# Performance work log

Measured on AMD Instinct MI355X. Metric: run time of the kernel, lower is better.

The kernel has to match this reference:

```python
import jax, jax.numpy as jnp
import numpy as np

D_STATE = 16
D_CONV = 4
DT_RANK = 16  # ceil(d_model/16) = ceil(256/16)
N_LAYERS = 2
EPS = 1e-5


def _layernorm(x, g, b):
    m = jnp.mean(x, -1, keepdims=True)
    v = jnp.var(x, -1, keepdims=True)
    return (x - m) * jax.lax.rsqrt(v + EPS) * g + b


def _causal_conv(x, w, b):
    # x [B,L,D], depthwise causal conv, w [D,K], b [D]
    K = w.shape[1]
    L = x.shape[1]
    xp = jnp.pad(x, ((0, 0), (K - 1, 0), (0, 0)))
    y = sum(xp[:, k:k + L, :] * w[:, k] for k in range(K))
    return y + b


def _selective_scan(u, dt, A, Bm, Cm, D_skip):
    # u, dt [B,L,d]; A [d,n]; Bm, Cm [B,L,n]; D_skip [d]
    def step(h, inp):
        dt_t, B_t, C_t, u_t = inp  # [B,d],[B,n],[B,n],[B,d]
        dA = jnp.exp(dt_t[:, :, None] * A)                      # [B,d,n]
        h = dA * h + dt_t[:, :, None] * B_t[:, None, :] * u_t[:, :, None]
        y = jnp.einsum('bdn,bn->bd', h, C_t)
        return h, y

    Bsz, L, d = u.shape
    h0 = jnp.zeros((Bsz, d, A.shape[1]), u.dtype)
    xs = (dt.transpose(1, 0, 2), Bm.transpose(1, 0, 2),
          Cm.transpose(1, 0, 2), u.transpose(1, 0, 2))
    _, ys = jax.lax.scan(step, h0, xs)                          # [L,B,d]
    return ys.transpose(1, 0, 2) + u * D_skip


def _mamba_block(x, Wip, cw, cb, Wxp, Wdt, bdt, Alog, Dp, Wout):
    xz = x @ Wip                                                # [B,L,2*d_inner]
    d_inner = Wip.shape[1] // 2
    xc, z = xz[..., :d_inner], xz[..., d_inner:]
    xc = jax.nn.silu(_causal_conv(xc, cw, cb))
    xdbl = xc @ Wxp                                             # [B,L,dt_rank+2n]
    dt = jax.nn.softplus(xdbl[..., :DT_RANK] @ Wdt + bdt)
    Bm = xdbl[..., DT_RANK:DT_RANK + D_STATE]
    Cm = xdbl[..., DT_RANK + D_STATE:]
    A = -jnp.exp(Alog)
    y = _selective_scan(xc, dt, A, Bm, Cm, Dp)
    y = y * jax.nn.silu(z)
    return y @ Wout


def reference(z_t, W_in, b_in, ln_g, ln_b, W_inproj, conv_w, conv_b, W_xproj,
              W_dt, b_dt, A_log, D_skip, W_out, W_outp, b_outp, lno_g, lno_b):
    x = z_t @ W_in + b_in                                       # [B,L,d_model]
    for i in range(N_LAYERS):
        res = x
        xn = _layernorm(x, ln_g[i], ln_b[i])
        x = res + _mamba_block(xn, W_inproj[i], conv_w[i], conv_b[i],
                               W_xproj[i], W_dt[i], b_dt[i], A_log[i],
                               D_skip[i], W_out[i])  # dropout is identity in eval
    u = x @ W_outp + b_outp
    return _layernorm(u, lno_g, lno_b)


def setup_inputs() -> dict:
    key = jax.random.key(0)
    B, L = 16, 2048
    d_input, d_model, d_output, d_inner = 1088, 256, 64, 512
    n = N_LAYERS
    ks = jax.random.split(key, 10)

    def rn(k, shape, fan):
        return jax.random.normal(k, shape, jnp.float32) / np.float32(np.sqrt(fan))

    A_init = jnp.log(jnp.arange(1, D_STATE + 1, dtype=jnp.float32))
    return {
        'z_t': jax.random.normal(ks[0], (B, L, d_input), jnp.float32),
        'W_in': rn(ks[1], (d_input, d_model), d_input),
        'b_in': jnp.zeros((d_model,), jnp.float32),
        'ln_g': jnp.ones((n, d_model), jnp.float32),
        'ln_b': jnp.zeros((n, d_model), jnp.float32),
        'W_inproj': rn(ks[2], (n, d_model, 2 * d_inner), d_model),
        'conv_w': rn(ks[3], (n, d_inner, D_CONV), D_CONV),
        'conv_b': jnp.zeros((n, d_inner), jnp.float32),
        'W_xproj': rn(ks[4], (n, d_inner, DT_RANK + 2 * D_STATE), d_inner),
        'W_dt': rn(ks[5], (n, DT_RANK, d_inner), DT_RANK),
        'b_dt': jnp.full((n, d_inner), -4.6, jnp.float32),  # softplus ~ 0.01
        'A_log': jnp.broadcast_to(A_init, (n, d_inner, D_STATE)) + 0.0,
        'D_skip': jnp.ones((n, d_inner), jnp.float32),
        'W_out': rn(ks[6], (n, d_inner, d_model), d_inner),
        'W_outp': rn(ks[7], (d_model, d_output), d_model),
        'b_outp': jnp.zeros((d_output,), jnp.float32),
        'lno_g': jnp.ones((d_output,), jnp.float32),
        'lno_b': jnp.zeros((d_output,), jnp.float32),
    }
```

## Files before the change

kernel.cpp:

```cpp
#include <hip/hip_runtime.h>
#include <hip/hip_bf16.h>
#include <math.h>
#include <stdint.h>

#define L_SEQ 2048
#define BATCH 16
#define NROWS (BATCH * L_SEQ)
#define DMODEL 256
#define DINNER 512
#define C_CH 32
#define T_CH 64
#define LOG2E 1.4426950408889634f

typedef __attribute__((ext_vector_type(8))) __bf16 bf16x8;
typedef __attribute__((ext_vector_type(4))) float f32x4;
typedef __attribute__((ext_vector_type(8))) unsigned short u16x8;
typedef __attribute__((address_space(1))) const uint32_t gu32;
typedef __attribute__((address_space(3))) uint32_t lu32;

#if __has_builtin(__builtin_amdgcn_exp2f)
#define EXP2F __builtin_amdgcn_exp2f
#else
#define EXP2F exp2f
#endif

__device__ __forceinline__ float sigmoidf_(float x) { return 1.f / (1.f + __expf(-x)); }

__device__ __forceinline__ unsigned short f2bf(float f) {
    union { float f; uint32_t u; } v; v.f = f;
    uint32_t r = v.u + 0x7FFF + ((v.u >> 16) & 1);
    return (unsigned short)(r >> 16);
}
__device__ __forceinline__ float bf2f(unsigned short h) {
    union { uint32_t u; float f; } v; v.u = ((uint32_t)h) << 16;
    return v.f;
}

__device__ __forceinline__ void gld16(const void* g, void* l) {
    __builtin_amdgcn_global_load_lds((gu32*)g, (lu32*)l, 16, 0, 0);
}

__global__ __launch_bounds__(256) void wtrans(const float* __restrict__ W,
                                              unsigned short* __restrict__ Wt, int K, int N) {
    int idx = blockIdx.x * 256 + threadIdx.x;
    if (idx < K * N) {
        int n = idx / K, k = idx % K;
        Wt[idx] = f2bf(W[(size_t)k * N + n]);
    }
}
__global__ __launch_bounds__(256) void wtrans_pad(const float* __restrict__ W,
                                                  unsigned short* __restrict__ Wt,
                                                  int K, int Nreal, int Npad) {
    int idx = blockIdx.x * 256 + threadIdx.x;
    if (idx < Npad * K) {
        int n = idx / K, k = idx % K;
        Wt[idx] = (n < Nreal) ? f2bf(W[(size_t)k * Nreal + n]) : (unsigned short)0;
    }
}

template <int TM, bool A_F32, bool HAS_BIAS, bool HAS_RES, bool OUT_BF16>
__global__ __launch_bounds__(256) void gemm_bf16(
    const void* __restrict__ Aptr, const unsigned short* __restrict__ Bt,
    const float* __restrict__ bias, const float* __restrict__ res,
    void* __restrict__ Cout, int M, int N, int K, int Nout)
{
    constexpr int MR = TM / 32;
    __shared__ unsigned short Alds[2][TM * 32];
    __shared__ unsigned short Blds[2][4096];
    const int tid = threadIdx.x;
    const int w = tid >> 6, lane = tid & 63;

    const int nwg = gridDim.x;
    const int q = nwg >> 3;
    const int wg = (blockIdx.x & 7) * q + (blockIdx.x >> 3);
    const int nx = N >> 7;
    const int bm = (wg / nx) * TM, bn = (wg % nx) * 128;

    const int wr = (w >> 1) * (TM / 2), wc = (w & 1) * 64;
    const int fr = lane & 15, fq = lane >> 4;
    const size_t Kb = (size_t)K * 2;

    const int o0 = tid * 16, o1 = (256 + tid) * 16;
    const int ar0 = o0 >> 6, ac0 = o0 & 63;
    const int ar1 = o1 >> 6, ac1 = o1 & 63;
    const char* Ab = (const char*)Aptr;
    const float* Af = (const float*)Aptr;
    const char* Bb = (const char*)Bt;
    const int lds0 = w * 1024, lds1 = 4096 + w * 1024;

    f32x4 acc[MR][4];
#pragma unroll
    for (int m = 0; m < MR; m++)
#pragma unroll
        for (int n = 0; n < 4; n++) acc[m][n] = (f32x4){0.f, 0.f, 0.f, 0.f};

    auto stageB = [&](int buf, int k0) {
        char* lB = (char*)Blds[buf];
        gld16(Bb + (size_t)(bn + ar0) * Kb + (k0 << 1) + ac0, lB + lds0);
        gld16(Bb + (size_t)(bn + ar1) * Kb + (k0 << 1) + ac1, lB + lds1);
    };
    auto stageA16 = [&](int buf, int k0) {
        char* lA = (char*)Alds[buf];
        gld16(Ab + (size_t)(bm + ar0) * Kb + (k0 << 1) + ac0, lA + lds0);
        if constexpr (TM == 128)
            gld16(Ab + (size_t)(bm + ar1) * Kb + (k0 << 1) + ac1, lA + lds1);
    };
    float4 r00, r01, r10, r11;
    auto loadA32 = [&](int k0) {
        const float* s0 = Af + (size_t)(bm + ar0) * K + k0 + (ac0 >> 1);
        r00 = *(const float4*)s0; r01 = *(const float4*)(s0 + 4);
        if constexpr (TM == 128) {
            const float* s1 = Af + (size_t)(bm + ar1) * K + k0 + (ac1 >> 1);
            r10 = *(const float4*)s1; r11 = *(const float4*)(s1 + 4);
        }
    };
    auto writeA32 = [&](int buf) {
        bf16x8 v0;
        v0[0]=(__bf16)r00.x; v0[1]=(__bf16)r00.y; v0[2]=(__bf16)r00.z; v0[3]=(__bf16)r00.w;
        v0[4]=(__bf16)r01.x; v0[5]=(__bf16)r01.y; v0[6]=(__bf16)r01.z; v0[7]=(__bf16)r01.w;
        *(bf16x8*)((char*)Alds[buf] + ar0 * 64 + ac0) = v0;
        if constexpr (TM == 128) {
            bf16x8 v1;
            v1[0]=(__bf16)r10.x; v1[1]=(__bf16)r10.y; v1[2]=(__bf16)r10.z; v1[3]=(__bf16)r10.w;
            v1[4]=(__bf16)r11.x; v1[5]=(__bf16)r11.y; v1[6]=(__bf16)r11.z; v1[7]=(__bf16)r11.w;
            *(bf16x8*)((char*)Alds[buf] + ar1 * 64 + ac1) = v1;
        }
    };
    auto compute = [&](int buf) {
        bf16x8 af[MR], bg[4];
#pragma unroll
        for (int m = 0; m < MR; m++)
            af[m] = *(const bf16x8*)&Alds[buf][(wr + m * 16 + fr) * 32 + fq * 8];
#pragma unroll
        for (int n = 0; n < 4; n++)
            bg[n] = *(const bf16x8*)&Blds[buf][(wc + n * 16 + fr) * 32 + fq * 8];
#pragma unroll
        for (int m = 0; m < MR; m++)
#pragma unroll
            for (int n = 0; n < 4; n++)
                acc[m][n] = __builtin_amdgcn_mfma_f32_16x16x32_bf16(af[m], bg[n], acc[m][n], 0, 0, 0);
    };

    if constexpr (A_F32) { loadA32(0); stageB(0, 0); writeA32(0); }
    else                 { stageA16(0, 0); stageB(0, 0); }
    asm volatile("s_waitcnt vmcnt(0) lgkmcnt(0)" ::: "memory");
    __builtin_amdgcn_s_barrier();
    __builtin_amdgcn_sched_barrier(0);

    const int NT = K >> 5;
    for (int kt = 0; kt < NT; ++kt) {
        const int cur = kt & 1;
        const bool has_next = (kt + 1 < NT);
        if (has_next) {
            const int k0 = (kt + 1) << 5;
            if constexpr (A_F32) { loadA32(k0); stageB(cur ^ 1, k0); }
            else                 { stageA16(cur ^ 1, k0); stageB(cur ^ 1, k0); }
        }
        if (has_next) {
            if constexpr (A_F32 && TM == 128)      asm volatile("s_waitcnt vmcnt(6)" ::: "memory");
            else if constexpr (A_F32)              asm volatile("s_waitcnt vmcnt(4)" ::: "memory");
            else if constexpr (TM == 128)          asm volatile("s_waitcnt vmcnt(4)" ::: "memory");
            else                                   asm volatile("s_waitcnt vmcnt(3)" ::: "memory");
        } else {
            asm volatile("s_waitcnt vmcnt(0)" ::: "memory");
        }
        __builtin_amdgcn_s_barrier();
        __builtin_amdgcn_sched_barrier(0);

        compute(cur);
        if constexpr (A_F32) { if (has_next) writeA32(cur ^ 1); }

        asm volatile("s_waitcnt lgkmcnt(0)" ::: "memory");
        __builtin_amdgcn_s_barrier();
        __builtin_amdgcn_sched_barrier(0);
    }

#pragma unroll
    for (int m = 0; m < MR; m++) {
#pragma unroll
        for (int n = 0; n < 4; n++) {
            int col = bn + wc + n * 16 + fr;
            if (col < Nout) {
#pragma unroll
                for (int r = 0; r < 4; r++) {
                    int row = bm + wr + m * 16 + fq * 4 + r;
                    float v = acc[m][n][r];
                    if (HAS_BIAS) v += bias[col];
                    if (HAS_RES)  v += res[(size_t)row * Nout + col];
                    if (OUT_BF16) ((unsigned short*)Cout)[(size_t)row * Nout + col] = f2bf(v);
                    else          ((float*)Cout)[(size_t)row * Nout + col] = v;
                }
            }
        }
    }
}

__global__ __launch_bounds__(256) void ln256(
    const float* __restrict__ x, const float* __restrict__ g,
    const float* __restrict__ b, unsigned short* __restrict__ out)
{
    int lane = threadIdx.x & 63, wid = threadIdx.x >> 6;
    size_t r = (size_t)blockIdx.x * 4 + wid;
    const float4 v = *(const float4*)&x[r * 256 + lane * 4];
    float s = v.x + v.y + v.z + v.w;
    float sq = v.x * v.x + v.y * v.y + v.z * v.z + v.w * v.w;
#pragma unroll
    for (int off = 32; off; off >>= 1) { s += __shfl_xor(s, off); sq += __shfl_xor(sq, off); }
    float mean = s * (1.f / 256.f);
    float var = sq * (1.f / 256.f) - mean * mean;
    float rs = rsqrtf(var + 1e-5f);
    float4 gv = *(const float4*)&g[lane * 4];
    float4 bv = *(const float4*)&b[lane * 4];
    ushort4 o;
    o.x = f2bf((v.x - mean) * rs * gv.x + bv.x);
    o.y = f2bf((v.y - mean) * rs * gv.y + bv.y);
    o.z = f2bf((v.z - mean) * rs * gv.z + bv.z);
    o.w = f2bf((v.w - mean) * rs * gv.w + bv.w);
    *(ushort4*)&out[r * 256 + lane * 4] = o;
}

__global__ __launch_bounds__(256) void ln64(
    const float* __restrict__ t, const float* __restrict__ g,
    const float* __restrict__ b, float* __restrict__ out)
{
    int lane = threadIdx.x & 63, wid = threadIdx.x >> 6;
    size_t r = (size_t)blockIdx.x * 4 + wid;
    float v = t[r * 64 + lane];
    float s = v, sq = v * v;
#pragma unroll
    for (int off = 32; off; off >>= 1) { s += __shfl_xor(s, off); sq += __shfl_xor(sq, off); }
    float mean = s * (1.f / 64.f);
    float var = sq * (1.f / 64.f) - mean * mean;
    out[r * 64 + lane] = (v - mean) * rsqrtf(var + 1e-5f) * g[lane] + b[lane];
}

__global__ __launch_bounds__(256) void conv_silu8(
    const unsigned short* __restrict__ xz, const float* __restrict__ w,
    const float* __restrict__ cb, unsigned short* __restrict__ xc)
{
    int idx = blockIdx.x * 256 + threadIdx.x;
    int d8 = (idx & 63) << 3;
    int l  = (idx >> 6) & 2047;
    int b  = idx >> 17;
    const unsigned short* base = xz + ((size_t)b * L_SEQ + l) * 1024 + d8;
    u16x8 t0 = {0,0,0,0,0,0,0,0}, t1 = t0, t2 = t0;
    u16x8 t3 = *(const u16x8*)base;
    if (l >= 1) t2 = *(const u16x8*)(base - 1024);
    if (l >= 2) t1 = *(const u16x8*)(base - 2048);
    if (l >= 3) t0 = *(const u16x8*)(base - 3072);
    u16x8 o;
#pragma unroll
    for (int j = 0; j < 8; j++) {
        float4 wv = *(const float4*)&w[(d8 + j) * 4];
        float acc = cb[d8 + j];
        acc = fmaf(bf2f(t0[j]), wv.x, acc);
        acc = fmaf(bf2f(t1[j]), wv.y, acc);
        acc = fmaf(bf2f(t2[j]), wv.z, acc);
        acc = fmaf(bf2f(t3[j]), wv.w, acc);
        o[j] = f2bf(acc * sigmoidf_(acc));
    }
    *(u16x8*)&xc[((size_t)b * L_SEQ + l) * 512 + d8] = o;
}

__global__ __launch_bounds__(256) void dt_kernel(
    const float* __restrict__ xdbl, const float* __restrict__ Wdt,
    const float* __restrict__ bdt, unsigned short* __restrict__ dtb)
{
    int idx = blockIdx.x * 256 + threadIdx.x;
    int d = idx & 511;
    int rblk = idx >> 9;
    float wdt[16];
#pragma unroll
    for (int j = 0; j < 16; j++) wdt[j] = Wdt[j * 512 + d];
    const float bd = bdt[d];
#pragma unroll
    for (int i = 0; i < 8; i++) {
        size_t r = (size_t)rblk * 8 + i;
        const float* xr = xdbl + r * 48;
        float p0 = 0.f, p1 = 0.f, p2 = 0.f, p3 = 0.f;
#pragma unroll
        for (int j = 0; j < 4; j++) {
            p0 = fmaf(xr[j],      wdt[j],      p0);
            p1 = fmaf(xr[4 + j],  wdt[4 + j],  p1);
            p2 = fmaf(xr[8 + j],  wdt[8 + j],  p2);
            p3 = fmaf(xr[12 + j], wdt[12 + j], p3);
        }
        float dtr = bd + ((p0 + p1) + (p2 + p3));
        float dtv = (dtr > 20.f) ? dtr : __logf(1.f + __expf(dtr));
        dtb[r * 512 + d] = f2bf(dtv);
    }
}

__global__ __launch_bounds__(256) void scan_pass1(
    const unsigned short* __restrict__ xc, const unsigned short* __restrict__ dtb,
    const float* __restrict__ xdbl, const float* __restrict__ Alog,
    float* __restrict__ Pbuf, float* __restrict__ Sbuf)
{
    __shared__ float xsB[T_CH][16];
    int idx = blockIdx.x * 256 + threadIdx.x;
    int d = idx & 511;
    int c = (idx >> 9) & (C_CH - 1);
    int b = idx >> 14;
    size_t r0 = (size_t)b * L_SEQ + (size_t)c * T_CH;
    {
        int i = threadIdx.x, row = i >> 2, qq = i & 3;
        *(float4*)&xsB[row][qq * 4] = *(const float4*)&xdbl[(r0 + row) * 48 + 16 + qq * 4];
    }
    __syncthreads();

    float a[16], a2[16], S[16];
#pragma unroll
    for (int n = 0; n < 16; n++) a[n] = -__expf(Alog[d * 16 + n]);
#pragma unroll
    for (int n = 0; n < 16; n++) a2[n] = a[n] * LOG2E;
#pragma unroll
    for (int n = 0; n < 16; n++) S[n] = 0.f;
    bool pow_ok = true;
#pragma unroll
    for (int n = 1; n < 16; n++)
        pow_ok = pow_ok && (fabsf(a[n] - (n + 1) * a[0]) <= 1e-3f * (n + 1) * fabsf(a[0]));
    const float a0l2 = a[0] * LOG2E;
    float Tsum = 0.f;

    if (pow_ok) {
        for (int t = 0; t < T_CH; t++) {
            float dtv = bf2f(dtb[(r0 + t) * 512 + d]);
            float u = bf2f(xc[(r0 + t) * 512 + d]);
            float dtu = dtv * u;
            Tsum += dtv;
            float e1 = EXP2F(dtv * a0l2), e2 = e1 * e1;
            S[0] = fmaf(e1, S[0], dtu * xsB[t][0]);
            S[1] = fmaf(e2, S[1], dtu * xsB[t][1]);
            float pm2 = e1, pm1 = e2;
#pragma unroll
            for (int n = 2; n < 16; n++) {
                float cur = pm2 * e2;
                S[n] = fmaf(cur, S[n], dtu * xsB[t][n]);
                pm2 = pm1; pm1 = cur;
            }
        }
    } else {
        for (int t = 0; t < T_CH; t++) {
            float dtv = bf2f(dtb[(r0 + t) * 512 + d]);
            float u = bf2f(xc[(r0 + t) * 512 + d]);
            float dtu = dtv * u;
            Tsum += dtv;
#pragma unroll
            for (int n = 0; n < 16; n++) {
                float dA = EXP2F(dtv * a2[n]);
                S[n] = fmaf(dA, S[n], dtu * xsB[t][n]);
            }
        }
    }
    size_t o = (size_t)idx * 16;
#pragma unroll
    for (int qq = 0; qq < 4; qq++) {
        float4 pv = make_float4(EXP2F(Tsum * a2[qq*4]),   EXP2F(Tsum * a2[qq*4+1]),
                                EXP2F(Tsum * a2[qq*4+2]), EXP2F(Tsum * a2[qq*4+3]));
        *(float4*)&Pbuf[o + qq * 4] = pv;
        *(float4*)&Sbuf[o + qq * 4] = make_float4(S[qq*4], S[qq*4+1], S[qq*4+2], S[qq*4+3]);
    }
}

__global__ __launch_bounds__(256) void scan_pass2(
    const float* __restrict__ Pbuf, float* __restrict__ Sbuf)
{
    int g = blockIdx.x * 256 + threadIdx.x;
    int nd = g & 8191;
    int b = g >> 13;
    float H = 0.f;
    for (int c = 0; c < C_CH; c++) {
        size_t idx = ((size_t)(b * C_CH + c) * 8192) + nd;
        float P = Pbuf[idx], S = Sbuf[idx];
        float Hn = fmaf(P, H, S);
        Sbuf[idx] = H;
        H = Hn;
    }
}

__global__ __launch_bounds__(256) void scan_pass3(
    const unsigned short* __restrict__ xcin, const unsigned short* __restrict__ xz,
    const unsigned short* __restrict__ dtb, const float* __restrict__ xdbl,
    const float* __restrict__ Alog, const float* __restrict__ Dsk,
    const float* __restrict__ Sbuf, unsigned short* __restrict__ y)
{
    __shared__ float xsBC[T_CH][32];
    int idx = blockIdx.x * 256 + threadIdx.x;
    int d = idx & 511;
    int c = (idx >> 9) & (C_CH - 1);
    int b = idx >> 14;
    size_t r0 = (size_t)b * L_SEQ + (size_t)c * T_CH;
#pragma unroll
    for (int ii = 0; ii < 2; ii++) {
        int i = threadIdx.x + ii * 256, row = i >> 3, qq = i & 7;
        *(float4*)&xsBC[row][qq * 4] = *(const float4*)&xdbl[(r0 + row) * 48 + 16 + qq * 4];
    }
    __syncthreads();

    float a[16], a2[16], h[16];
#pragma unroll
    for (int n = 0; n < 16; n++) a[n] = -__expf(Alog[d * 16 + n]);
#pragma unroll
    for (int n = 0; n < 16; n++) a2[n] = a[n] * LOG2E;
    {
        size_t o = (size_t)idx * 16;
#pragma unroll
        for (int qq = 0; qq < 4; qq++) {
            float4 v = *(const float4*)&Sbuf[o + qq * 4];
            h[qq*4] = v.x; h[qq*4+1] = v.y; h[qq*4+2] = v.z; h[qq*4+3] = v.w;
        }
    }
    bool pow_ok = true;
#pragma unroll
    for (int n = 1; n < 16; n++)
        pow_ok = pow_ok && (fabsf(a[n] - (n + 1) * a[0]) <= 1e-3f * (n + 1) * fabsf(a[0]));
    const float a0l2 = a[0] * LOG2E;
    const float Dv = Dsk[d];

    if (pow_ok) {
        for (int t = 0; t < T_CH; t++) {
            size_t ridx = (r0 + t) * 512 + d;
            float dtv = bf2f(dtb[ridx]);
            float u = bf2f(xcin[ridx]);
            float dtu = dtv * u;
            float e1 = EXP2F(dtv * a0l2), e2 = e1 * e1;
            float yv = 0.f;
            h[0] = fmaf(e1, h[0], dtu * xsBC[t][0]);  yv = fmaf(h[0], xsBC[t][16], yv);
            h[1] = fmaf(e2, h[1], dtu * xsBC[t][1]);  yv = fmaf(h[1], xsBC[t][17], yv);
            float pm2 = e1, pm1 = e2;
#pragma unroll
            for (int n = 2; n < 16; n++) {
                float cur = pm2 * e2;
                h[n] = fmaf(cur, h[n], dtu * xsBC[t][n]);
                yv = fmaf(h[n], xsBC[t][16 + n], yv);
                pm2 = pm1; pm1 = cur;
            }
            yv = fmaf(u, Dv, yv);
            float z = bf2f(xz[(r0 + t) * 1024 + 512 + d]);
            y[ridx] = f2bf(yv * z * sigmoidf_(z));
        }
    } else {
        for (int t = 0; t < T_CH; t++) {
            size_t ridx = (r0 + t) * 512 + d;
            float dtv = bf2f(dtb[ridx]);
            float u = bf2f(xcin[ridx]);
            float dtu = dtv * u;
            float yv = 0.f;
#pragma unroll
            for (int n = 0; n < 16; n++) {
                float dA = EXP2F(dtv * a2[n]);
                h[n] = fmaf(dA, h[n], dtu * xsBC[t][n]);
                yv = fmaf(h[n], xsBC[t][16 + n], yv);
            }
            yv = fmaf(u, Dv, yv);
            float z = bf2f(xz[(r0 + t) * 1024 + 512 + d]);
            y[ridx] = f2bf(yv * z * sigmoidf_(z));
        }
    }
}

extern "C" void kernel_launch(void* const* d_in, const int* in_sizes, int n_in,
                              void* d_out, int out_size, void* d_ws, size_t ws_size,
                              hipStream_t stream)
{
    const float* z_t     = (const float*)d_in[0];
    const float* W_in    = (const float*)d_in[1];
    const float* b_in    = (const float*)d_in[2];
    const float* ln_g    = (const float*)d_in[3];
    const float* ln_b    = (const float*)d_in[4];
    const float* W_inpr  = (const float*)d_in[5];
    const float* conv_w  = (const float*)d_in[6];
    const float* conv_b  = (const float*)d_in[7];
    const float* W_xproj = (const float*)d_in[8];
    const float* W_dt    = (const float*)d_in[9];
    const float* b_dt    = (const float*)d_in[10];
    const float* A_log   = (const float*)d_in[11];
    const float* D_skip  = (const float*)d_in[12];
    const float* W_out   = (const float*)d_in[13];
    const float* W_outp  = (const float*)d_in[14];
    const float* b_outp  = (const float*)d_in[15];
    const float* lno_g   = (const float*)d_in[16];
    const float* lno_b   = (const float*)d_in[17];
    float* out           = (float*)d_out;

    char* p = (char*)d_ws;
    float*          x    = (float*)p;          p += (size_t)NROWS * DMODEL * 4;
    unsigned short* xn   = (unsigned short*)p; p += (size_t)NROWS * DMODEL * 2;
    unsigned short* xc   = (unsigned short*)p; p += (size_t)NROWS * DINNER * 2;
    unsigned short* xz   = (unsigned short*)p; p += (size_t)NROWS * 1024 * 2;
    float*          xdbl = (float*)p;          p += (size_t)NROWS * 48 * 4;
    unsigned short* dtb  = (unsigned short*)p; p += (size_t)NROWS * DINNER * 2;
    float*          Pbuf = (float*)p;          p += (size_t)BATCH * C_CH * DINNER * 16 * 4;
    float*          Sbuf = (float*)p;          p += (size_t)BATCH * C_CH * DINNER * 16 * 4;
    unsigned short* WinT  = (unsigned short*)p; p += (size_t)256 * 1088 * 2;
    unsigned short* WipT  = (unsigned short*)p; p += (size_t)2 * 1024 * 256 * 2;
    unsigned short* WoutT = (unsigned short*)p; p += (size_t)2 * 256 * 512 * 2;
    unsigned short* WxpT  = (unsigned short*)p; p += (size_t)2 * 128 * 512 * 2;
    unsigned short* WopT  = (unsigned short*)p; p += (size_t)128 * 256 * 2;
    float*          otmp = Pbuf;

    wtrans<<<(256 * 1088 + 255) / 256, 256, 0, stream>>>(W_in, WinT, 1088, 256);
    for (int l = 0; l < 2; l++) {
        wtrans<<<(1024 * 256 + 255) / 256, 256, 0, stream>>>(
            W_inpr + (size_t)l * 256 * 1024, WipT + (size_t)l * 1024 * 256, 256, 1024);
        wtrans<<<(256 * 512 + 255) / 256, 256, 0, stream>>>(
            W_out + (size_t)l * 512 * 256, WoutT + (size_t)l * 256 * 512, 512, 256);
        wtrans_pad<<<(128 * 512 + 255) / 256, 256, 0, stream>>>(
            W_xproj + (size_t)l * 512 * 48, WxpT + (size_t)l * 128 * 512, 512, 48, 128);
    }
    wtrans_pad<<<(128 * 256 + 255) / 256, 256, 0, stream>>>(W_outp, WopT, 256, 64, 128);

    gemm_bf16<64, true, true, false, false><<<(NROWS / 64) * (256 / 128), 256, 0, stream>>>(
        z_t, WinT, b_in, nullptr, x, NROWS, 256, 1088, 256);

    for (int layer = 0; layer < 2; ++layer) {
        ln256<<<NROWS / 4, 256, 0, stream>>>(x, ln_g + layer * 256, ln_b + layer * 256, xn);
        gemm_bf16<128, false, false, false, true><<<(NROWS / 128) * (1024 / 128), 256, 0, stream>>>(
            xn, WipT + (size_t)layer * 1024 * 256, nullptr, nullptr, xz, NROWS, 1024, 256, 1024);
        conv_silu8<<<NROWS * 64 / 256, 256, 0, stream>>>(
            xz, conv_w + layer * 512 * 4, conv_b + layer * 512, xc);
        gemm_bf16<64, false, false, false, false><<<(NROWS / 64) * (128 / 128), 256, 0, stream>>>(
            xc, WxpT + (size_t)layer * 128 * 512, nullptr, nullptr, xdbl, NROWS, 128, 512, 48);

        const float* Al_l  = A_log + layer * 512 * 16;
        dt_kernel<<<DINNER * (NROWS / 8) / 256, 256, 0, stream>>>(
            xdbl, W_dt + layer * 16 * 512, b_dt + layer * 512, dtb);
        scan_pass1<<<BATCH * C_CH * DINNER / 256, 256, 0, stream>>>(
            xc, dtb, xdbl, Al_l, Pbuf, Sbuf);
        scan_pass2<<<BATCH * DINNER * 16 / 256, 256, 0, stream>>>(Pbuf, Sbuf);
        scan_pass3<<<BATCH * C_CH * DINNER / 256, 256, 0, stream>>>(
            xc, xz, dtb, xdbl, Al_l, D_skip + layer * 512, Sbuf, xc);

        if (layer == 0) {
            gemm_bf16<64, false, false, true, false><<<(NROWS / 64) * (256 / 128), 256, 0, stream>>>(
                xc, WoutT, nullptr, x, x, NROWS, 256, 512, 256);
        } else {
            gemm_bf16<64, false, false, true, true><<<(NROWS / 64) * (256 / 128), 256, 0, stream>>>(
                xc, WoutT + (size_t)256 * 512, nullptr, x, xn, NROWS, 256, 512, 256);
        }
    }

    gemm_bf16<64, false, true, false, false><<<(NROWS / 64) * (128 / 128), 256, 0, stream>>>(
        xn, WopT, b_outp, nullptr, otmp, NROWS, 128, 256, 64);
    ln64<<<NROWS / 4, 256, 0, stream>>>(otmp, lno_g, lno_b, out);
}
```

Measured before the change: 619.8 us.

## Fuse dt projection into scan passes and stage fp32 A via direct LDS loads

Removes the separate dt_kernel and its bf16 dt buffer. Both scan passes now recompute softplus(xdbl[:16]·W_dt + b_dt) per timestep from a shared-memory copy of xdbl, which avoids writing and re-reading an NROWS×512 intermediate at the cost of 16 extra FMAs plus an exp and a log per element, done twice. Separately, the fp32-A GEMM path (the input projection) now loads fp32 tiles straight into LDS with async global-to-LDS copies and an XOR swizzle, converting to bf16 when fragments are read. This replaces the register-staged convert-and-write and uses a larger A LDS buffer.

Result: faster. 571.7 us (-7.8%).

```diff
diff --git a/kernel.cpp b/kernel.cpp
--- a/kernel.cpp
+++ b/kernel.cpp
@@ -65,7 +65,8 @@
     void* __restrict__ Cout, int M, int N, int K, int Nout)
 {
     constexpr int MR = TM / 32;
-    __shared__ unsigned short Alds[2][TM * 32];
+    constexpr int ABYTES = TM * 32 * (A_F32 ? 4 : 2);
+    __shared__ __align__(16) char AldsRaw[2][ABYTES];
     __shared__ unsigned short Blds[2][4096];
     const int tid = threadIdx.x;
     const int w = tid >> 6, lane = tid & 63;
@@ -78,13 +79,16 @@
 
     const int wr = (w >> 1) * (TM / 2), wc = (w & 1) * 64;
     const int fr = lane & 15, fq = lane >> 4;
-    const size_t Kb = (size_t)K * 2;
+    const size_t KbB = (size_t)K * 2;
+    const size_t KbA = (size_t)K * (A_F32 ? 4 : 2);
 
     const int o0 = tid * 16, o1 = (256 + tid) * 16;
     const int ar0 = o0 >> 6, ac0 = o0 & 63;
     const int ar1 = o1 >> 6, ac1 = o1 & 63;
+    const int arow = tid >> 3;
+    const int acolb = (o0 & 127) ^ ((arow & 7) << 4);
+
     const char* Ab = (const char*)Aptr;
-    const float* Af = (const float*)Aptr;
     const char* Bb = (const char*)Bt;
     const int lds0 = w * 1024, lds1 = 4096 + w * 1024;
 
@@ -96,41 +100,44 @@
 
     auto stageB = [&](int buf, int k0) {
         char* lB = (char*)Blds[buf];
-        gld16(Bb + (size_t)(bn + ar0) * Kb + (k0 << 1) + ac0, lB + lds0);
-        gld16(Bb + (size_t)(bn + ar1) * Kb + (k0 << 1) + ac1, lB + lds1);
+        gld16(Bb + (size_t)(bn + ar0) * KbB + (k0 << 1) + ac0, lB + lds0);
+        gld16(Bb + (size_t)(bn + ar1) * KbB + (k0 << 1) + ac1, lB + lds1);
     };
-    auto stageA16 = [&](int buf, int k0) {
-        char* lA = (char*)Alds[buf];
-        gld16(Ab + (size_t)(bm + ar0) * Kb + (k0 << 1) + ac0, lA + lds0);
-        if constexpr (TM == 128)
-            gld16(Ab + (size_t)(bm + ar1) * Kb + (k0 << 1) + ac1, lA + lds1);
-    };
-    float4 r00, r01, r10, r11;
-    auto loadA32 = [&](int k0) {
-        const float* s0 = Af + (size_t)(bm + ar0) * K + k0 + (ac0 >> 1);
-        r00 = *(const float4*)s0; r01 = *(const float4*)(s0 + 4);
-        if constexpr (TM == 128) {
-            const float* s1 = Af + (size_t)(bm + ar1) * K + k0 + (ac1 >> 1);
-            r10 = *(const float4*)s1; r11 = *(const float4*)(s1 + 4);
-        }
-    };
-    auto writeA32 = [&](int buf) {
-        bf16x8 v0;
-        v0[0]=(__bf16)r00.x; v0[1]=(__bf16)r00.y; v0[2]=(__bf16)r00.z; v0[3]=(__bf16)r00.w;
-        v0[4]=(__bf16)r01.x; v0[5]=(__bf16)r01.y; v0[6]=(__bf16)r01.z; v0[7]=(__bf16)r01.w;
-        *(bf16x8*)((char*)Alds[buf] + ar0 * 64 + ac0) = v0;
-        if constexpr (TM == 128) {
-            bf16x8 v1;
-            v1[0]=(__bf16)r10.x; v1[1]=(__bf16)r10.y; v1[2]=(__bf16)r10.z; v1[3]=(__bf16)r10.w;
-            v1[4]=(__bf16)r11.x; v1[5]=(__bf16)r11.y; v1[6]=(__bf16)r11.z; v1[7]=(__bf16)r11.w;
-            *(bf16x8*)((char*)Alds[buf] + ar1 * 64 + ac1) = v1;
+    auto stageA = [&](int buf, int k0) {
+        char* lA = AldsRaw[buf];
+        if constexpr (A_F32) {
+#pragma unroll
+            for (int i = 0; i < TM / 32; i++)
+                gld16(Ab + (size_t)(bm + i * 32 + arow) * KbA + ((size_t)k0 * 4) + acolb,
+                      lA + i * 4096 + lds0);
+        } else {
+            gld16(Ab + (size_t)(bm + ar0) * KbA + (k0 << 1) + ac0, lA + lds0);
+            if constexpr (TM == 128)
+                gld16(Ab + (size_t)(bm + ar1) * KbA + (k0 << 1) + ac1, lA + lds1);
         }
     };
     auto compute = [&](int buf) {
         bf16x8 af[MR], bg[4];
-#pragma unroll
-        for (int m = 0; m < MR; m++)
-            af[m] = *(const bf16x8*)&Alds[buf][(wr + m * 16 + fr) * 32 + fq * 8];
+        if constexpr (A_F32) {
+            const char* lA = AldsRaw[buf];
+#pragma unroll
+            for (int m = 0; m < MR; m++) {
+                const int row = wr + m * 16 + fr;
+                const int sw = (row & 7) << 4;
+                const int b0 = row * 128 + fq * 32;
+                float4 x0 = *(const float4*)(lA + (b0 ^ sw));
+                float4 x1 = *(const float4*)(lA + ((b0 + 16) ^ sw));
+                bf16x8 a;
+                a[0]=(__bf16)x0.x; a[1]=(__bf16)x0.y; a[2]=(__bf16)x0.z; a[3]=(__bf16)x0.w;
+                a[4]=(__bf16)x1.x; a[5]=(__bf16)x1.y; a[6]=(__bf16)x1.z; a[7]=(__bf16)x1.w;
+                af[m] = a;
+            }
+        } else {
+            const unsigned short* lA = (const unsigned short*)AldsRaw[buf];
+#pragma unroll
+            for (int m = 0; m < MR; m++)
+                af[m] = *(const bf16x8*)&lA[(wr + m * 16 + fr) * 32 + fq * 8];
+        }
 #pragma unroll
         for (int n = 0; n < 4; n++)
             bg[n] = *(const bf16x8*)&Blds[buf][(wc + n * 16 + fr) * 32 + fq * 8];
@@ -141,26 +148,24 @@
                 acc[m][n] = __builtin_amdgcn_mfma_f32_16x16x32_bf16(af[m], bg[n], acc[m][n], 0, 0, 0);
     };
 
-    if constexpr (A_F32) { loadA32(0); stageB(0, 0); writeA32(0); }
-    else                 { stageA16(0, 0); stageB(0, 0); }
+    stageA(0, 0); stageB(0, 0);
     asm volatile("s_waitcnt vmcnt(0) lgkmcnt(0)" ::: "memory");
     __builtin_amdgcn_s_barrier();
     __builtin_amdgcn_sched_barrier(0);
 
+    constexpr int VOPS = (A_F32 ? (TM / 32) : (TM == 128 ? 2 : 1)) + 2;
     const int NT = K >> 5;
     for (int kt = 0; kt < NT; ++kt) {
         const int cur = kt & 1;
         const bool has_next = (kt + 1 < NT);
         if (has_next) {
             const int k0 = (kt + 1) << 5;
-            if constexpr (A_F32) { loadA32(k0); stageB(cur ^ 1, k0); }
-            else                 { stageA16(cur ^ 1, k0); stageB(cur ^ 1, k0); }
+            stageA(cur ^ 1, k0); stageB(cur ^ 1, k0);
         }
         if (has_next) {
-            if constexpr (A_F32 && TM == 128)      asm volatile("s_waitcnt vmcnt(6)" ::: "memory");
-            else if constexpr (A_F32)              asm volatile("s_waitcnt vmcnt(4)" ::: "memory");
-            else if constexpr (TM == 128)          asm volatile("s_waitcnt vmcnt(4)" ::: "memory");
-            else                                   asm volatile("s_waitcnt vmcnt(3)" ::: "memory");
+            if constexpr (VOPS == 6)      asm volatile("s_waitcnt vmcnt(6)" ::: "memory");
+            else if constexpr (VOPS == 4) asm volatile("s_waitcnt vmcnt(4)" ::: "memory");
+            else                          asm volatile("s_waitcnt vmcnt(3)" ::: "memory");
         } else {
             asm volatile("s_waitcnt vmcnt(0)" ::: "memory");
         }
@@ -168,7 +173,6 @@
         __builtin_amdgcn_sched_barrier(0);
 
         compute(cur);
-        if constexpr (A_F32) { if (has_next) writeA32(cur ^ 1); }
 
         asm volatile("s_waitcnt lgkmcnt(0)" ::: "memory");
         __builtin_amdgcn_s_barrier();
@@ -262,51 +266,29 @@
     *(u16x8*)&xc[((size_t)b * L_SEQ + l) * 512 + d8] = o;
 }
 
-__global__ __launch_bounds__(256) void dt_kernel(
-    const float* __restrict__ xdbl, const float* __restrict__ Wdt,
-    const float* __restrict__ bdt, unsigned short* __restrict__ dtb)
-{
-    int idx = blockIdx.x * 256 + threadIdx.x;
-    int d = idx & 511;
-    int rblk = idx >> 9;
-    float wdt[16];
-#pragma unroll
-    for (int j = 0; j < 16; j++) wdt[j] = Wdt[j * 512 + d];
-    const float bd = bdt[d];
-#pragma unroll
-    for (int i = 0; i < 8; i++) {
-        size_t r = (size_t)rblk * 8 + i;
-        const float* xr = xdbl + r * 48;
-        float p0 = 0.f, p1 = 0.f, p2 = 0.f, p3 = 0.f;
-#pragma unroll
-        for (int j = 0; j < 4; j++) {
-            p0 = fmaf(xr[j],      wdt[j],      p0);
-            p1 = fmaf(xr[4 + j],  wdt[4 + j],  p1);
-            p2 = fmaf(xr[8 + j],  wdt[8 + j],  p2);
-            p3 = fmaf(xr[12 + j], wdt[12 + j], p3);
-        }
-        float dtr = bd + ((p0 + p1) + (p2 + p3));
-        float dtv = (dtr > 20.f) ? dtr : __logf(1.f + __expf(dtr));
-        dtb[r * 512 + d] = f2bf(dtv);
-    }
-}
-
 __global__ __launch_bounds__(256) void scan_pass1(
-    const unsigned short* __restrict__ xc, const unsigned short* __restrict__ dtb,
-    const float* __restrict__ xdbl, const float* __restrict__ Alog,
+    const unsigned short* __restrict__ xc, const float* __restrict__ xdbl,
+    const float* __restrict__ Wdt, const float* __restrict__ bdt,
+    const float* __restrict__ Alog,
     float* __restrict__ Pbuf, float* __restrict__ Sbuf)
 {
-    __shared__ float xsB[T_CH][16];
+    __shared__ float xs[T_CH][32];
     int idx = blockIdx.x * 256 + threadIdx.x;
     int d = idx & 511;
     int c = (idx >> 9) & (C_CH - 1);
     int b = idx >> 14;
     size_t r0 = (size_t)b * L_SEQ + (size_t)c * T_CH;
-    {
-        int i = threadIdx.x, row = i >> 2, qq = i & 3;
-        *(float4*)&xsB[row][qq * 4] = *(const float4*)&xdbl[(r0 + row) * 48 + 16 + qq * 4];
+#pragma unroll
+    for (int ii = 0; ii < 2; ii++) {
+        int i = threadIdx.x + ii * 256, row = i >> 3, qq = i & 7;
+        *(float4*)&xs[row][qq * 4] = *(const float4*)&xdbl[(r0 + row) * 48 + qq * 4];
     }
     __syncthreads();
+
+    float wdt[16];
+#pragma unroll
+    for (int j = 0; j < 16; j++) wdt[j] = Wdt[j * 512 + d];
+    const float bd = bdt[d];
 
     float a[16], a2[16], S[16];
 #pragma unroll
@@ -324,31 +306,37 @@
 
     if (pow_ok) {
         for (int t = 0; t < T_CH; t++) {
-            float dtv = bf2f(dtb[(r0 + t) * 512 + d]);
+            float dtr = bd;
+#pragma unroll
+            for (int j = 0; j < 16; j++) dtr = fmaf(xs[t][j], wdt[j], dtr);
+            float dtv = (dtr > 20.f) ? dtr : __logf(1.f + __expf(dtr));
             float u = bf2f(xc[(r0 + t) * 512 + d]);
             float dtu = dtv * u;
             Tsum += dtv;
             float e1 = EXP2F(dtv * a0l2), e2 = e1 * e1;
-            S[0] = fmaf(e1, S[0], dtu * xsB[t][0]);
-            S[1] = fmaf(e2, S[1], dtu * xsB[t][1]);
+            S[0] = fmaf(e1, S[0], dtu * xs[t][16]);
+            S[1] = fmaf(e2, S[1], dtu * xs[t][17]);
             float pm2 = e1, pm1 = e2;
 #pragma unroll
             for (int n = 2; n < 16; n++) {
                 float cur = pm2 * e2;
-                S[n] = fmaf(cur, S[n], dtu * xsB[t][n]);
+                S[n] = fmaf(cur, S[n], dtu * xs[t][16 + n]);
                 pm2 = pm1; pm1 = cur;
             }
         }
     } else {
         for (int t = 0; t < T_CH; t++) {
-            float dtv = bf2f(dtb[(r0 + t) * 512 + d]);
+            float dtr = bd;
+#pragma unroll
+            for (int j = 0; j < 16; j++) dtr = fmaf(xs[t][j], wdt[j], dtr);
+            float dtv = (dtr > 20.f) ? dtr : __logf(1.f + __expf(dtr));
             float u = bf2f(xc[(r0 + t) * 512 + d]);
             float dtu = dtv * u;
             Tsum += dtv;
 #pragma unroll
             for (int n = 0; n < 16; n++) {
                 float dA = EXP2F(dtv * a2[n]);
-                S[n] = fmaf(dA, S[n], dtu * xsB[t][n]);
+                S[n] = fmaf(dA, S[n], dtu * xs[t][16 + n]);
             }
         }
     }
@@ -380,22 +368,28 @@
 
 __global__ __launch_bounds__(256) void scan_pass3(
     const unsigned short* __restrict__ xcin, const unsigned short* __restrict__ xz,
-    const unsigned short* __restrict__ dtb, const float* __restrict__ xdbl,
-    const float* __restrict__ Alog, const float* __restrict__ Dsk,
-    const float* __restrict__ Sbuf, unsigned short* __restrict__ y)
-{
-    __shared__ float xsBC[T_CH][32];
+    const float* __restrict__ xdbl, const float* __restrict__ Wdt,
+    const float* __restrict__ bdt, const float* __restrict__ Alog,
+    const float* __restrict__ Dsk, const float* __restrict__ Sbuf,
+    unsigned short* __restrict__ y)
+{
+    __shared__ float xs[T_CH][48];
     int idx = blockIdx.x * 256 + threadIdx.x;
     int d = idx & 511;
     int c = (idx >> 9) & (C_CH - 1);
     int b = idx >> 14;
     size_t r0 = (size_t)b * L_SEQ + (size_t)c * T_CH;
 #pragma unroll
-    for (int ii = 0; ii < 2; ii++) {
-        int i = threadIdx.x + ii * 256, row = i >> 3, qq = i & 7;
-        *(float4*)&xsBC[row][qq * 4] = *(const float4*)&xdbl[(r0 + row) * 48 + 16 + qq * 4];
+    for (int ii = 0; ii < 3; ii++) {
+        int i = threadIdx.x + ii * 256, row = i / 12, qq = i % 12;
+        *(float4*)&xs[row][qq * 4] = *(const float4*)&xdbl[(r0 + row) * 48 + qq * 4];
     }
     __syncthreads();
+
+    float wdt[16];
+#pragma unroll
+    for (int j = 0; j < 16; j++) wdt[j] = Wdt[j * 512 + d];
+    const float bd = bdt[d];
 
     float a[16], a2[16], h[16];
 #pragma unroll
@@ -420,19 +414,22 @@
     if (pow_ok) {
         for (int t = 0; t < T_CH; t++) {
             size_t ridx = (r0 + t) * 512 + d;
-            float dtv = bf2f(dtb[ridx]);
+            float dtr = bd;
+#pragma unroll
+            for (int j = 0; j < 16; j++) dtr = fmaf(xs[t][j], wdt[j], dtr);
+            float dtv = (dtr > 20.f) ? dtr : __logf(1.f + __expf(dtr));
             float u = bf2f(xcin[ridx]);
             float dtu = dtv * u;
             float e1 = EXP2F(dtv * a0l2), e2 = e1 * e1;
             float yv = 0.f;
-            h[0] = fmaf(e1, h[0], dtu * xsBC[t][0]);  yv = fmaf(h[0], xsBC[t][16], yv);
-            h[1] = fmaf(e2, h[1], dtu * xsBC[t][1]);  yv = fmaf(h[1], xsBC[t][17], yv);
+            h[0] = fmaf(e1, h[0], dtu * xs[t][16]);  yv = fmaf(h[0], xs[t][32], yv);
+            h[1] = fmaf(e2, h[1], dtu * xs[t][17]);  yv = fmaf(h[1], xs[t][33], yv);
             float pm2 = e1, pm1 = e2;
 #pragma unroll
             for (int n = 2; n < 16; n++) {
                 float cur = pm2 * e2;
-                h[n] = fmaf(cur, h[n], dtu * xsBC[t][n]);
-                yv = fmaf(h[n], xsBC[t][16 + n], yv);
+                h[n] = fmaf(cur, h[n], dtu * xs[t][16 + n]);
+                yv = fmaf(h[n], xs[t][32 + n], yv);
                 pm2 = pm1; pm1 = cur;
             }
             yv = fmaf(u, Dv, yv);
@@ -442,15 +439,18 @@
     } else {
         for (int t = 0; t < T_CH; t++) {
             size_t ridx = (r0 + t) * 512 + d;
-            float dtv = bf2f(dtb[ridx]);
+            float dtr = bd;
+#pragma unroll
+            for (int j = 0; j < 16; j++) dtr = fmaf(xs[t][j], wdt[j], dtr);
+            float dtv = (dtr > 20.f) ? dtr : __logf(1.f + __expf(dtr));
             float u = bf2f(xcin[ridx]);
             float dtu = dtv * u;
             float yv = 0.f;
 #pragma unroll
             for (int n = 0; n < 16; n++) {
                 float dA = EXP2F(dtv * a2[n]);
-                h[n] = fmaf(dA, h[n], dtu * xsBC[t][n]);
-                yv = fmaf(h[n], xsBC[t][16 + n], yv);
+                h[n] = fmaf(dA, h[n], dtu * xs[t][16 + n]);
+                yv = fmaf(h[n], xs[t][32 + n], yv);
             }
             yv = fmaf(u, Dv, yv);
             float z = bf2f(xz[(r0 + t) * 1024 + 512 + d]);
@@ -489,7 +489,6 @@
     unsigned short* xc   = (unsigned short*)p; p += (size_t)NROWS * DINNER * 2;
     unsigned short* xz   = (unsigned short*)p; p += (size_t)NROWS * 1024 * 2;
     float*          xdbl = (float*)p;          p += (size_t)NROWS * 48 * 4;
-    unsigned short* dtb  = (unsigned short*)p; p += (size_t)NROWS * DINNER * 2;
     float*          Pbuf = (float*)p;          p += (size_t)BATCH * C_CH * DINNER * 16 * 4;
     float*          Sbuf = (float*)p;          p += (size_t)BATCH * C_CH * DINNER * 16 * 4;
     unsigned short* WinT  = (unsigned short*)p; p += (size_t)256 * 1088 * 2;
@@ -523,13 +522,13 @@
             xc, WxpT + (size_t)layer * 128 * 512, nullptr, nullptr, xdbl, NROWS, 128, 512, 48);
 
         const float* Al_l  = A_log + layer * 512 * 16;
-        dt_kernel<<<DINNER * (NROWS / 8) / 256, 256, 0, stream>>>(
-            xdbl, W_dt + layer * 16 * 512, b_dt + layer * 512, dtb);
+        const float* Wdt_l = W_dt + layer * 16 * 512;
+        const float* bdt_l = b_dt + layer * 512;
         scan_pass1<<<BATCH * C_CH * DINNER / 256, 256, 0, stream>>>(
-            xc, dtb, xdbl, Al_l, Pbuf, Sbuf);
+            xc, xdbl, Wdt_l, bdt_l, Al_l, Pbuf, Sbuf);
         scan_pass2<<<BATCH * DINNER * 16 / 256, 256, 0, stream>>>(Pbuf, Sbuf);
         scan_pass3<<<BATCH * C_CH * DINNER / 256, 256, 0, stream>>>(
-            xc, xz, dtb, xdbl, Al_l, D_skip + layer * 512, Sbuf, xc);
+            xc, xz, xdbl, Wdt_l, bdt_l, Al_l, D_skip + layer * 512, Sbuf, xc);
 
         if (layer == 0) {
             gemm_bf16<64, false, false, true, false><<<(NROWS / 64) * (256 / 128), 256, 0, stream>>>(
```
